# Optimization experiments

Hardware: AMD Instinct MI355X
Metric: run time of the kernel (lower is better)

Reference implementation:

```python
import jax, jax.numpy as jnp
import numpy as np

NUM_EMB = 1024
EMB_DIM = 256
COMMIT = 0.25
EPS = 1e-12  # matches torch F.normalize eps


def _l2norm(x):
    return x / jnp.maximum(jnp.linalg.norm(x, axis=-1, keepdims=True), EPS)


def setup_inputs() -> dict:
    key = jax.random.key(0)
    k1, k2 = jax.random.split(key)
    inputs = jax.random.normal(k1, (64, 256, 32, 32), dtype=jnp.float32)
    weight = jax.random.uniform(k2, (NUM_EMB, EMB_DIM), dtype=jnp.float32,
                                minval=-1.0 / NUM_EMB, maxval=1.0 / NUM_EMB)
    return {"inputs": inputs, "weight": weight}


def reference(inputs, weight):
    B, D, H, W = inputs.shape
    x = jnp.transpose(inputs, (0, 2, 3, 1))           # [B,H,W,D]
    flat = x.reshape(-1, D)                           # [N,D]
    fn = _l2norm(flat)                                # normalized inputs
    wn = _l2norm(weight)                              # normalized codebook [K,D]
    # squared euclidean distances between unit vectors
    dist = (jnp.sum(fn * fn, axis=1, keepdims=True)
            + jnp.sum(wn * wn, axis=1)
            - 2.0 * fn @ wn.T)                        # [N,K]
    idx = jnp.argmin(dist, axis=1)                    # [N]
    quant = wn[idx].reshape(x.shape)                  # codebook gather == onehot @ wn
    inorm = fn.reshape(x.shape)
    e_loss = jnp.mean((jax.lax.stop_gradient(quant) - inorm) ** 2)
    q_loss = jnp.mean((quant - jax.lax.stop_gradient(inorm)) ** 2)
    loss = q_loss + COMMIT * e_loss
    quant_st = inorm + jax.lax.stop_gradient(quant - inorm)  # straight-through
    return loss, jnp.transpose(quant_st, (0, 3, 1, 2)), idx[:, None]
```

## Files before the change

### kernel.cpp

```cpp
#include <hip/hip_runtime.h>
#include <math.h>

#define NUM_EMB 1024
#define EMB_DIM 256
#define N_ROWS  65536
#define HW      1024
#define QUANT_OFF 1
#define IDX_OFF   (1 + 16777216)
#define LDA 264
#define KSTR 132

typedef unsigned int uint;
typedef _Float16 f16x8 __attribute__((ext_vector_type(8)));
typedef float    f32x4 __attribute__((ext_vector_type(4)));

__device__ __forceinline__ uint umin2(uint a, uint b) { return a < b ? a : b; }
__device__ __forceinline__ uint umax2(uint a, uint b) { return a > b ? a : b; }

__device__ __forceinline__ uint umed3(uint a, uint b, uint c) {
  uint d;
  asm("v_med3_u32 %0, %1, %2, %3" : "=v"(d) : "v"(a), "v"(b), "v"(c));
  return d;
}

__global__ __launch_bounds__(256)
void k_norm_w(const float* __restrict__ w, float* __restrict__ wn,
              _Float16* __restrict__ wh2, double* __restrict__ rinv) {
  const int k = blockIdx.x, t = threadIdx.x;
  const float v = w[(size_t)k * EMB_DIM + t];
  double s = (double)v * (double)v;
  for (int o = 32; o; o >>= 1) s += __shfl_down(s, o);
  __shared__ double ps[4];
  if ((t & 63) == 0) ps[t >> 6] = s;
  __syncthreads();
  const double tot = ps[0] + ps[1] + ps[2] + ps[3];
  const float nv = v / fmaxf((float)sqrt(tot), 1e-12f);
  wn[(size_t)k * EMB_DIM + t] = nv;
  const int chunk = k >> 8, cc = k & 255;
  const int ks = t >> 5, q = (t >> 3) & 3, e = t & 7;
  wh2[(size_t)chunk * 65536 + ks * 8192 + q * 2048 + cc * 8 + e] = (_Float16)nv;
  if (t == 0) rinv[k] = 1.0 / fmax(sqrt(tot), 1e-12);
}

__global__ __launch_bounds__(256, 3)
void k_pass1(const float* __restrict__ x, const _Float16* __restrict__ wh2,
             uint* __restrict__ cand) {
  __shared__ __align__(16) _Float16 As[64 * LDA];
  const int t = threadIdx.x;
  const int blk = blockIdx.x;
  const int b = blk >> 4;
  const int hw0 = (blk & 15) * 64;

  const int lane = t & 63;
  const int q = lane >> 4;
  const int l15 = lane & 15;
  const int w = t >> 6;

  const int bvo0 = q * 2048 + (w * 64 +  0 + l15) * 8;
  const int bvo1 = q * 2048 + (w * 64 + 16 + l15) * 8;
  const int bvo2 = q * 2048 + (w * 64 + 32 + l15) * 8;
  const int bvo3 = q * 2048 + (w * 64 + 48 + l15) * 8;

#define LOADB(buf, cc, kk)                                            \
  { const _Float16* ksb_ = wh2 + (size_t)((cc) * 8 + (kk)) * 8192;    \
    buf[0] = *(const f16x8*)&ksb_[bvo0];                              \
    buf[1] = *(const f16x8*)&ksb_[bvo1];                              \
    buf[2] = *(const f16x8*)&ksb_[bvo2];                              \
    buf[3] = *(const f16x8*)&ksb_[bvo3]; }

  f16x8 bb[2][4];
  LOADB(bb[0], 0, 0);

  {
    const int r = t & 63;
    const int ph = t >> 6;
    const float* xb = x + (size_t)b * (EMB_DIM * HW) + hw0 + r;
#pragma unroll
    for (int jp = 0; jp < 8; ++jp) {
      const int d0 = ph * 64 + jp * 8;
      f16x8 v;
#pragma unroll
      for (int e = 0; e < 8; ++e)
        v[e] = (_Float16)xb[(size_t)(d0 + e) * HW];
      *(f16x8*)&As[r * LDA + d0] = v;
    }
  }
  __syncthreads();

  uint t1[16], t2[16];
#pragma unroll
  for (int i = 0; i < 16; ++i) { t1[i] = 0u; t2[i] = 0u; }

#pragma unroll
  for (int c4 = 0; c4 < 4; ++c4) {
    f32x4 acc[4][4];
#pragma unroll
    for (int rt = 0; rt < 4; ++rt)
#pragma unroll
      for (int ct = 0; ct < 4; ++ct) acc[rt][ct] = (f32x4)0.f;

#pragma unroll
    for (int ks = 0; ks < 8; ++ks) {
      const int cb = ks & 1, nb = cb ^ 1;
      if (ks < 7) { LOADB(bb[nb], c4, ks + 1); }
      else if (c4 < 3) { LOADB(bb[nb], c4 + 1, 0); }

      const f16x8 a0 = *(const f16x8*)&As[(0 * 16 + l15) * LDA + ks * 32 + q * 8];
      const f16x8 a1 = *(const f16x8*)&As[(1 * 16 + l15) * LDA + ks * 32 + q * 8];
      const f16x8 a2 = *(const f16x8*)&As[(2 * 16 + l15) * LDA + ks * 32 + q * 8];
      const f16x8 a3 = *(const f16x8*)&As[(3 * 16 + l15) * LDA + ks * 32 + q * 8];

      __builtin_amdgcn_s_setprio(1);
#pragma unroll
      for (int ct = 0; ct < 4; ++ct) {
        acc[0][ct] = __builtin_amdgcn_mfma_f32_16x16x32_f16(a0, bb[cb][ct], acc[0][ct], 0, 0, 0);
        acc[1][ct] = __builtin_amdgcn_mfma_f32_16x16x32_f16(a1, bb[cb][ct], acc[1][ct], 0, 0, 0);
        acc[2][ct] = __builtin_amdgcn_mfma_f32_16x16x32_f16(a2, bb[cb][ct], acc[2][ct], 0, 0, 0);
        acc[3][ct] = __builtin_amdgcn_mfma_f32_16x16x32_f16(a3, bb[cb][ct], acc[3][ct], 0, 0, 0);
      }
      __builtin_amdgcn_s_setprio(0);
    }

#pragma unroll
    for (int ct = 0; ct < 4; ++ct) {
      const uint idxv = (uint)(c4 * 256 + w * 64 + ct * 16 + l15);
#pragma unroll
      for (int rt = 0; rt < 4; ++rt)
#pragma unroll
        for (int r = 0; r < 4; ++r) {
          const float v = fmaxf(acc[rt][ct][r], 0.0f);
          const uint key = (__float_as_uint(v) & 0xFFFFFC00u) | idxv;
          const int slot = rt * 4 + r;
          t2[slot] = umed3(key, t1[slot], t2[slot]);
          t1[slot] = umax2(key, t1[slot]);
        }
    }
  }
#undef LOADB

  __syncthreads();
  uint* keys = (uint*)As;
#pragma unroll
  for (int slot = 0; slot < 16; ++slot) {
    const int rt = slot >> 2, r = slot & 3;
    const int row = rt * 16 + q * 4 + r;
    const int col = w * 32 + l15 * 2;
    keys[row * KSTR + col] = t1[slot];
    keys[row * KSTR + col + 1] = t2[slot];
  }
  __syncthreads();
  {
    const int row = t >> 2, seg = t & 3;
    uint s1 = 0, s2 = 0;
#pragma unroll
    for (int i = 0; i < 8; ++i) {
      const int ii = (i + t) & 7;
      const uint4 k4 = *(const uint4*)&keys[row * KSTR + seg * 32 + ii * 4];
      const uint kk[4] = {k4.x, k4.y, k4.z, k4.w};
#pragma unroll
      for (int e = 0; e < 4; ++e) {
        s2 = umed3(kk[e], s1, s2);
        s1 = umax2(kk[e], s1);
      }
    }
    __syncthreads();
    keys[t * 2] = s1;
    keys[t * 2 + 1] = s2;
  }
  __syncthreads();
  if (t < 64) {
    uint c0 = 0, c1 = 0, c2 = 0, c3 = 0;
#pragma unroll
    for (int i = 0; i < 8; ++i) {
      const uint k = keys[t * 8 + i];
      const uint n0 = umin2(c0, k); c0 = umax2(c0, k);
      const uint n1 = umin2(c1, n0); c1 = umax2(c1, n0);
      const uint n2 = umin2(c2, n1); c2 = umax2(c2, n1);
      c3 = umax2(c3, n2);
    }
    uint4 o; o.x = c0; o.y = c1; o.z = c2; o.w = c3;
    *(uint4*)&cand[(size_t)(blk * 64 + t) * 4] = o;
  }
}

#define XSTR 257
__global__ __launch_bounds__(256)
void k_finish(const float* __restrict__ x, const float* __restrict__ w,
              const float* __restrict__ wn, const double* __restrict__ rinv,
              const uint* __restrict__ cand, float* __restrict__ out) {
  __shared__ float smem[256 * 33];
  __shared__ double lsum[4];
  const int t = threadIdx.x;
  const int blk = blockIdx.x;
  const int b = blk >> 5;
  const int hw0 = (blk & 31) * 32;

  {
    const int r = t & 31, dp = t >> 5;
    const float* xb = x + (size_t)b * (EMB_DIM * HW) + hw0 + r;
#pragma unroll
    for (int j = 0; j < 32; ++j) {
      const int d = dp * 32 + j;
      smem[r * XSTR + d] = xb[(size_t)d * HW];
    }
  }
  __syncthreads();

  const int row = t >> 3;
  const int li = t & 7;
  const int n0 = blk * 32 + row;
  const uint4 ck = *(const uint4*)&cand[(size_t)n0 * 4];
  const uint cv[4] = {ck.x, ck.y, ck.z, ck.w};

  float xf[32];
#pragma unroll
  for (int k = 0; k < 8; ++k)
#pragma unroll
    for (int e = 0; e < 4; ++e)
      xf[k * 4 + e] = smem[row * XSTR + k * 32 + li * 4 + e];
  __syncthreads();

  double sxx = 0.0;
#pragma unroll
  for (int i = 0; i < 32; ++i) sxx = fma((double)xf[i], (double)xf[i], sxx);

  double sj[4];
#pragma unroll
  for (int j = 0; j < 4; ++j) {
    const int c = (int)(cv[j] & 1023u);
    const float* wr = w + (size_t)c * EMB_DIM;
    double s = 0.0;
#pragma unroll
    for (int k = 0; k < 8; ++k) {
      const float4 w4 = *(const float4*)&wr[k * 32 + li * 4];
      const float wv[4] = {w4.x, w4.y, w4.z, w4.w};
#pragma unroll
      for (int e = 0; e < 4; ++e)
        s = fma((double)xf[k * 4 + e], (double)wv[e], s);
    }
    sj[j] = s;
  }

#pragma unroll
  for (int o = 4; o; o >>= 1) {
    sxx += __shfl_down(sxx, o);
#pragma unroll
    for (int j = 0; j < 4; ++j) sj[j] += __shfl_down(sj[j], o);
  }

  double dmin = 0.0;
  int cw = 0;
  if (li == 0) {
    double qbest = -1e300; cw = 1 << 30;
#pragma unroll
    for (int j = 0; j < 4; ++j) {
      const int c = (int)(cv[j] & 1023u);
      const double qj = sj[j] * rinv[c];
      if (qj > qbest || (qj == qbest && c < cw)) { qbest = qj; cw = c; }
    }
    dmin = 2.0 - 2.0 * qbest / fmax(sqrt(sxx), 1e-12);
    out[IDX_OFF + n0] = (float)cw;
  }
  cw = __shfl(cw, (t & 63) & ~7);

  double v = dmin;
  v += __shfl_down(v, 32);
  v += __shfl_down(v, 16);
  v += __shfl_down(v, 8);
  if ((t & 63) == 0) lsum[t >> 6] = v;
  __syncthreads();
  if (t == 0)
    atomicAdd(out, (float)(1.25 * (lsum[0] + lsum[1] + lsum[2] + lsum[3]) / 16777216.0));

  {
    const float* wr = wn + (size_t)cw * EMB_DIM;
#pragma unroll
    for (int k = 0; k < 8; ++k) {
      const int d0 = k * 32 + li * 4;
      const float4 w4 = *(const float4*)&wr[d0];
      smem[(d0 + 0) * 33 + row] = w4.x;
      smem[(d0 + 1) * 33 + row] = w4.y;
      smem[(d0 + 2) * 33 + row] = w4.z;
      smem[(d0 + 3) * 33 + row] = w4.w;
    }
  }
  __syncthreads();
  {
    const int hw4 = (t & 7) * 4, dbase = t >> 3;
    float* qout = out + QUANT_OFF + (size_t)b * (EMB_DIM * HW) + hw0;
#pragma unroll
    for (int jj = 0; jj < 8; ++jj) {
      const int d = jj * 32 + dbase;
      float4 v4;
      v4.x = smem[d * 33 + hw4 + 0];
      v4.y = smem[d * 33 + hw4 + 1];
      v4.z = smem[d * 33 + hw4 + 2];
      v4.w = smem[d * 33 + hw4 + 3];
      *(float4*)&qout[(size_t)d * HW + hw4] = v4;
    }
  }
}

extern "C" void kernel_launch(void* const* d_in, const int* in_sizes, int n_in,
                              void* d_out, int out_size, void* d_ws, size_t ws_size,
                              hipStream_t stream) {
  const float* x = (const float*)d_in[0];
  const float* w = (const float*)d_in[1];
  float* out = (float*)d_out;

  char* ws = (char*)d_ws;
  float*     wn   = (float*)ws;
  _Float16*  wh2  = (_Float16*)(ws + 1048576);
  double*    rinv = (double*)(ws + 1048576 + 524288);
  uint*      cand = (uint*)(ws + 1048576 + 524288 + 8192);

  hipMemsetAsync(d_out, 0, sizeof(float), stream);
  hipLaunchKernelGGL(k_norm_w, dim3(NUM_EMB), dim3(256), 0, stream, w, wn, wh2, rinv);
  hipLaunchKernelGGL(k_pass1, dim3(N_ROWS / 64), dim3(256), 0, stream, x, wh2, cand);
  hipLaunchKernelGGL(k_finish, dim3(N_ROWS / 32), dim3(256), 0, stream, x, w, wn, rinv, cand, out);
}
```

Before: 185.9 us.

## Fuse candidate selection and fp64 rescoring into one kernel

Merges the MFMA candidate pass and the finish pass into one kernel. Each thread keeps its fp32 slice of x in 64 registers, so the exact fp64 rescoring of the top-4 candidates reuses those values instead of re-reading x from global memory. The candidate list stays in shared memory rather than a workspace buffer, and quantized outputs are written in two 32-row halves. The cost is much higher register pressure, with launch bounds lowered from 3 to 2 blocks per CU, which reduces occupancy for the MFMA phase.

```diff
diff --git a/kernel.cpp b/kernel.cpp
--- a/kernel.cpp
+++ b/kernel.cpp
@@ -42,10 +42,13 @@
   if (t == 0) rinv[k] = 1.0 / fmax(sqrt(tot), 1e-12);
 }
 
-__global__ __launch_bounds__(256, 3)
-void k_pass1(const float* __restrict__ x, const _Float16* __restrict__ wh2,
-             uint* __restrict__ cand) {
+__global__ __launch_bounds__(256, 2)
+void k_fused(const float* __restrict__ x, const _Float16* __restrict__ wh2,
+             const float* __restrict__ w, const float* __restrict__ wn,
+             const double* __restrict__ rinv, float* __restrict__ out) {
   __shared__ __align__(16) _Float16 As[64 * LDA];
+  __shared__ uint4 cand_s[64];
+  __shared__ int   cw_s[64];
   const int t = threadIdx.x;
   const int blk = blockIdx.x;
   const int b = blk >> 4;
@@ -54,12 +57,12 @@
   const int lane = t & 63;
   const int q = lane >> 4;
   const int l15 = lane & 15;
-  const int w = t >> 6;
-
-  const int bvo0 = q * 2048 + (w * 64 +  0 + l15) * 8;
-  const int bvo1 = q * 2048 + (w * 64 + 16 + l15) * 8;
-  const int bvo2 = q * 2048 + (w * 64 + 32 + l15) * 8;
-  const int bvo3 = q * 2048 + (w * 64 + 48 + l15) * 8;
+  const int w4id = t >> 6;
+
+  const int bvo0 = q * 2048 + (w4id * 64 +  0 + l15) * 8;
+  const int bvo1 = q * 2048 + (w4id * 64 + 16 + l15) * 8;
+  const int bvo2 = q * 2048 + (w4id * 64 + 32 + l15) * 8;
+  const int bvo3 = q * 2048 + (w4id * 64 + 48 + l15) * 8;
 
 #define LOADB(buf, cc, kk)                                            \
   { const _Float16* ksb_ = wh2 + (size_t)((cc) * 8 + (kk)) * 8192;    \
@@ -71,18 +74,22 @@
   f16x8 bb[2][4];
   LOADB(bb[0], 0, 0);
 
+  const int r_own = t & 63;
+  const int ph = t >> 6;
+  float xv[64];
   {
-    const int r = t & 63;
-    const int ph = t >> 6;
-    const float* xb = x + (size_t)b * (EMB_DIM * HW) + hw0 + r;
+    const float* xb = x + (size_t)b * (EMB_DIM * HW) + hw0 + r_own;
 #pragma unroll
     for (int jp = 0; jp < 8; ++jp) {
       const int d0 = ph * 64 + jp * 8;
       f16x8 v;
 #pragma unroll
-      for (int e = 0; e < 8; ++e)
-        v[e] = (_Float16)xb[(size_t)(d0 + e) * HW];
-      *(f16x8*)&As[r * LDA + d0] = v;
+      for (int e = 0; e < 8; ++e) {
+        const float f = xb[(size_t)(d0 + e) * HW];
+        xv[jp * 8 + e] = f;
+        v[e] = (_Float16)f;
+      }
+      *(f16x8*)&As[r_own * LDA + d0] = v;
     }
   }
   __syncthreads();
@@ -123,7 +130,7 @@
 
 #pragma unroll
     for (int ct = 0; ct < 4; ++ct) {
-      const uint idxv = (uint)(c4 * 256 + w * 64 + ct * 16 + l15);
+      const uint idxv = (uint)(c4 * 256 + w4id * 64 + ct * 16 + l15);
 #pragma unroll
       for (int rt = 0; rt < 4; ++rt)
 #pragma unroll
@@ -144,7 +151,7 @@
   for (int slot = 0; slot < 16; ++slot) {
     const int rt = slot >> 2, r = slot & 3;
     const int row = rt * 16 + q * 4 + r;
-    const int col = w * 32 + l15 * 2;
+    const int col = w4id * 32 + l15 * 2;
     keys[row * KSTR + col] = t1[slot];
     keys[row * KSTR + col + 1] = t2[slot];
   }
@@ -179,125 +186,103 @@
       c3 = umax2(c3, n2);
     }
     uint4 o; o.x = c0; o.y = c1; o.z = c2; o.w = c3;
-    *(uint4*)&cand[(size_t)(blk * 64 + t) * 4] = o;
-  }
-}
-
-#define XSTR 257
-__global__ __launch_bounds__(256)
-void k_finish(const float* __restrict__ x, const float* __restrict__ w,
-              const float* __restrict__ wn, const double* __restrict__ rinv,
-              const uint* __restrict__ cand, float* __restrict__ out) {
-  __shared__ float smem[256 * 33];
-  __shared__ double lsum[4];
-  const int t = threadIdx.x;
-  const int blk = blockIdx.x;
-  const int b = blk >> 5;
-  const int hw0 = (blk & 31) * 32;
-
+    cand_s[t] = o;
+  }
+  __syncthreads();
+
+  double* red = (double*)As;
   {
-    const int r = t & 31, dp = t >> 5;
-    const float* xb = x + (size_t)b * (EMB_DIM * HW) + hw0 + r;
-#pragma unroll
-    for (int j = 0; j < 32; ++j) {
-      const int d = dp * 32 + j;
-      smem[r * XSTR + d] = xb[(size_t)d * HW];
-    }
-  }
-  __syncthreads();
-
-  const int row = t >> 3;
-  const int li = t & 7;
-  const int n0 = blk * 32 + row;
-  const uint4 ck = *(const uint4*)&cand[(size_t)n0 * 4];
-  const uint cv[4] = {ck.x, ck.y, ck.z, ck.w};
-
-  float xf[32];
-#pragma unroll
-  for (int k = 0; k < 8; ++k)
-#pragma unroll
-    for (int e = 0; e < 4; ++e)
-      xf[k * 4 + e] = smem[row * XSTR + k * 32 + li * 4 + e];
-  __syncthreads();
-
-  double sxx = 0.0;
-#pragma unroll
-  for (int i = 0; i < 32; ++i) sxx = fma((double)xf[i], (double)xf[i], sxx);
-
-  double sj[4];
-#pragma unroll
-  for (int j = 0; j < 4; ++j) {
-    const int c = (int)(cv[j] & 1023u);
-    const float* wr = w + (size_t)c * EMB_DIM;
-    double s = 0.0;
-#pragma unroll
-    for (int k = 0; k < 8; ++k) {
-      const float4 w4 = *(const float4*)&wr[k * 32 + li * 4];
-      const float wv[4] = {w4.x, w4.y, w4.z, w4.w};
-#pragma unroll
-      for (int e = 0; e < 4; ++e)
-        s = fma((double)xf[k * 4 + e], (double)wv[e], s);
-    }
-    sj[j] = s;
-  }
-
-#pragma unroll
-  for (int o = 4; o; o >>= 1) {
-    sxx += __shfl_down(sxx, o);
-#pragma unroll
-    for (int j = 0; j < 4; ++j) sj[j] += __shfl_down(sj[j], o);
-  }
-
-  double dmin = 0.0;
-  int cw = 0;
-  if (li == 0) {
-    double qbest = -1e300; cw = 1 << 30;
+    const uint4 ck = cand_s[r_own];
+    const uint cv[4] = {ck.x, ck.y, ck.z, ck.w};
+    double sxx_p = 0.0;
+#pragma unroll
+    for (int i = 0; i < 64; ++i) sxx_p = fma((double)xv[i], (double)xv[i], sxx_p);
+#pragma unroll
+    for (int j = 0; j < 4; ++j) {
+      const int c = (int)(cv[j] & 1023u);
+      const float* wr = w + (size_t)c * EMB_DIM + ph * 64;
+      double s = 0.0;
+#pragma unroll
+      for (int k = 0; k < 16; ++k) {
+        const float4 wv = *(const float4*)&wr[k * 4];
+        s = fma((double)xv[k * 4 + 0], (double)wv.x, s);
+        s = fma((double)xv[k * 4 + 1], (double)wv.y, s);
+        s = fma((double)xv[k * 4 + 2], (double)wv.z, s);
+        s = fma((double)xv[k * 4 + 3], (double)wv.w, s);
+      }
+      red[t * 5 + j] = s;
+    }
+    red[t * 5 + 4] = sxx_p;
+  }
+  __syncthreads();
+
+  if (t < 64) {
+    const uint4 ck = cand_s[t];
+    const uint cv[4] = {ck.x, ck.y, ck.z, ck.w};
+    double sj[4] = {0.0, 0.0, 0.0, 0.0};
+    double sxx = 0.0;
+#pragma unroll
+    for (int p = 0; p < 4; ++p) {
+      const int base = (p * 64 + t) * 5;
+      sj[0] += red[base + 0];
+      sj[1] += red[base + 1];
+      sj[2] += red[base + 2];
+      sj[3] += red[base + 3];
+      sxx   += red[base + 4];
+    }
+    double qbest = -1e300; int cw = 1 << 30;
 #pragma unroll
     for (int j = 0; j < 4; ++j) {
       const int c = (int)(cv[j] & 1023u);
       const double qj = sj[j] * rinv[c];
       if (qj > qbest || (qj == qbest && c < cw)) { qbest = qj; cw = c; }
     }
-    dmin = 2.0 - 2.0 * qbest / fmax(sqrt(sxx), 1e-12);
-    out[IDX_OFF + n0] = (float)cw;
-  }
-  cw = __shfl(cw, (t & 63) & ~7);
-
-  double v = dmin;
-  v += __shfl_down(v, 32);
-  v += __shfl_down(v, 16);
-  v += __shfl_down(v, 8);
-  if ((t & 63) == 0) lsum[t >> 6] = v;
-  __syncthreads();
-  if (t == 0)
-    atomicAdd(out, (float)(1.25 * (lsum[0] + lsum[1] + lsum[2] + lsum[3]) / 16777216.0));
-
-  {
+    const double dmin = 2.0 - 2.0 * qbest / fmax(sqrt(sxx), 1e-12);
+    out[IDX_OFF + blk * 64 + t] = (float)cw;
+    cw_s[t] = cw;
+    double v = dmin;
+    v += __shfl_down(v, 32);
+    v += __shfl_down(v, 16);
+    v += __shfl_down(v, 8);
+    v += __shfl_down(v, 4);
+    v += __shfl_down(v, 2);
+    v += __shfl_down(v, 1);
+    if (t == 0)
+      atomicAdd(out, (float)(1.25 * v / 16777216.0));
+  }
+  __syncthreads();
+
+  float* qs = (float*)As;
+  const int rw = t >> 3, li = t & 7;
+#pragma unroll 1
+  for (int half = 0; half < 2; ++half) {
+    const int cw = cw_s[half * 32 + rw];
     const float* wr = wn + (size_t)cw * EMB_DIM;
 #pragma unroll
     for (int k = 0; k < 8; ++k) {
       const int d0 = k * 32 + li * 4;
-      const float4 w4 = *(const float4*)&wr[d0];
-      smem[(d0 + 0) * 33 + row] = w4.x;
-      smem[(d0 + 1) * 33 + row] = w4.y;
-      smem[(d0 + 2) * 33 + row] = w4.z;
-      smem[(d0 + 3) * 33 + row] = w4.w;
-    }
-  }
-  __syncthreads();
-  {
-    const int hw4 = (t & 7) * 4, dbase = t >> 3;
-    float* qout = out + QUANT_OFF + (size_t)b * (EMB_DIM * HW) + hw0;
-#pragma unroll
-    for (int jj = 0; jj < 8; ++jj) {
-      const int d = jj * 32 + dbase;
-      float4 v4;
-      v4.x = smem[d * 33 + hw4 + 0];
-      v4.y = smem[d * 33 + hw4 + 1];
-      v4.z = smem[d * 33 + hw4 + 2];
-      v4.w = smem[d * 33 + hw4 + 3];
-      *(float4*)&qout[(size_t)d * HW + hw4] = v4;
-    }
+      const float4 wv = *(const float4*)&wr[d0];
+      qs[(d0 + 0) * 33 + rw] = wv.x;
+      qs[(d0 + 1) * 33 + rw] = wv.y;
+      qs[(d0 + 2) * 33 + rw] = wv.z;
+      qs[(d0 + 3) * 33 + rw] = wv.w;
+    }
+    __syncthreads();
+    {
+      const int hw4 = (t & 7) * 4, dbase = t >> 3;
+      float* qout = out + QUANT_OFF + (size_t)b * (EMB_DIM * HW) + hw0 + half * 32;
+#pragma unroll
+      for (int jj = 0; jj < 8; ++jj) {
+        const int d = jj * 32 + dbase;
+        float4 v4;
+        v4.x = qs[d * 33 + hw4 + 0];
+        v4.y = qs[d * 33 + hw4 + 1];
+        v4.z = qs[d * 33 + hw4 + 2];
+        v4.w = qs[d * 33 + hw4 + 3];
+        *(float4*)&qout[(size_t)d * HW + hw4] = v4;
+      }
+    }
+    __syncthreads();
   }
 }
 
@@ -312,10 +297,8 @@
   float*     wn   = (float*)ws;
   _Float16*  wh2  = (_Float16*)(ws + 1048576);
   double*    rinv = (double*)(ws + 1048576 + 524288);
-  uint*      cand = (uint*)(ws + 1048576 + 524288 + 8192);
 
   hipMemsetAsync(d_out, 0, sizeof(float), stream);
   hipLaunchKernelGGL(k_norm_w, dim3(NUM_EMB), dim3(256), 0, stream, w, wn, wh2, rinv);
-  hipLaunchKernelGGL(k_pass1, dim3(N_ROWS / 64), dim3(256), 0, stream, x, wh2, cand);
-  hipLaunchKernelGGL(k_finish, dim3(N_ROWS / 32), dim3(256), 0, stream, x, w, wn, rinv, cand, out);
+  hipLaunchKernelGGL(k_fused, dim3(N_ROWS / 64), dim3(256), 0, stream, x, wh2, w, wn, rinv, out);
 }
```

Result: no change. 185.4 us (-0.3%).
